# Optimization experiments

Measured on AMD Instinct MI355X. Metric: run time of the kernel, lower is better.

Reference implementation:

```python
import jax, jax.numpy as jnp
import numpy as np

N = 8192   # num_nodes
H = 128    # hidden_dim
B = 100    # batch of events
K = 5      # num_neg_samples
TD_MAX = 10000.0
TIME_SD = jnp.array([50.0, 7.0, 15.0, 15.0])  # time_sd from forward; time_mean = 0


def setup_inputs() -> dict:
    key = jax.random.key(0)
    ks = jax.random.split(key, 16)
    p = 32.0 / N  # avg degree ~32
    A = (jax.random.uniform(ks[0], (N, N)) < p).astype(jnp.float32)
    # S init: S[v,u] = 1/D[v] for neighbors u (row-normalized A)
    S = A / (A.sum(axis=1, keepdims=True) + 1e-7)
    z0 = jax.random.normal(ks[1], (N, H)) * 0.1
    u = jax.random.randint(ks[2], (B,), 0, N)
    v = jax.random.randint(ks[3], (B,), 0, N)
    event_types = jax.random.randint(ks[4], (B,), 0, 2)
    neg_idx = jax.random.randint(ks[5], (B, 2 * K), 0, N)
    time_diff = jax.random.normal(ks[6], (B, 2, 4))
    t_bar = jax.random.uniform(ks[7], (B, N)) * 1000.0
    t = 1000.0 + 10.0 * jnp.arange(B, dtype=jnp.float32)

    def lin(k, o, i):
        k1, k2 = jax.random.split(k)
        lim = 1.0 / np.sqrt(i)
        return (jax.random.uniform(k1, (o, i), minval=-lim, maxval=lim),
                jax.random.uniform(k2, (o,), minval=-lim, maxval=lim))

    om0_w, om0_b = lin(ks[8], 1, 2 * H)
    om1_w, om1_b = lin(ks[9], 1, 2 * H)
    Wh_w, Wh_b = lin(ks[10], H, H)
    Ws_w, Ws_b = lin(ks[11], H, H)
    Wr_w, Wr_b = lin(ks[12], H, H)
    Wt_w, Wt_b = lin(ks[13], H, 4)
    return dict(u=u, v=v, event_types=event_types, neg_idx=neg_idx,
                time_diff=time_diff, t_bar=t_bar, t=t, z0=z0, A=A, S=S,
                w_t=0.5 * jnp.ones(2), alpha=0.5 * jnp.ones(2), psi=0.5 * jnp.ones(2),
                om0_w=om0_w, om0_b=om0_b, om1_w=om1_w, om1_b=om1_b,
                Wh_w=Wh_w, Wh_b=Wh_b, Ws_w=Ws_w, Ws_b=Ws_b,
                Wr_w=Wr_w, Wr_b=Wr_b, Wt_w=Wt_w, Wt_b=Wt_b)


def _forward(u, v, event_types, neg_idx, time_diff, t_bar, t, z0, A, S,
             w_t, alpha, psi, om0_w, om0_b, om1_w, om1_b,
             Wh_w, Wh_b, Ws_w, Ws_b, Wr_w, Wr_b, Wt_w, Wt_b):
    td_norm = time_diff / TIME_SD  # (td - 0) / sd

    def hawkes(zu, zv, et, td):
        # lambda = psi * log(1 + exp(g/psi)) + alpha * exp(-w_t * td/td_max)
        zc = jnp.concatenate([zu, zv], axis=-1)
        g0 = jnp.einsum('...d,d->...', zc, om0_w[0]) + om0_b[0]
        g1 = jnp.einsum('...d,d->...', zc, om1_w[0]) + om1_b[0]
        g = jnp.where(et == 0, g0, g1)
        ps, al, wt = psi[et], alpha[et], w_t[et]
        gp = jnp.clip(g / (ps + 1e-7), -75.0, 75.0)
        return ps * jnp.log1p(jnp.exp(gp)) + al * jnp.exp(-wt * (td / TD_MAX))

    ar = jnp.arange(N)

    def step(z, ev):
        u_it, v_it, et, td2, tb, t_it, neg = ev
        z_u, z_v = z[u_it], z[v_it]
        Wh_all = z @ Wh_w.T + Wh_b  # [N,H]

        def struct(node):
            # structural attention over node's neighbors (masked, not dense loop)
            mask = A[node] > 0
            q = jnp.exp(S[node]) * mask
            q = q / (q.sum() + 1e-7)
            hsig = jax.nn.sigmoid(q[:, None] * Wh_all)
            hmax = jnp.where(mask[:, None], hsig, -jnp.inf).max(axis=0)
            return jnp.where(jnp.any(mask), hmax, 0.0)

        # update of u uses struct info from v's neighborhood, and vice versa
        hs = jnp.stack([struct(v_it), struct(u_it)])  # [2,H]
        h = (hs @ Ws_w.T + Ws_b) + (jnp.stack([z_u, z_v]) @ Wr_w.T + Wr_b) + (td2 @ Wt_w.T + Wt_b)
        z_upd = jax.nn.sigmoid(h)
        z_new = z.at[u_it].set(z_upd[0]).at[v_it].set(z_upd[1])

        # negative pairs: (u, v_neg_k) then (u_neg_k, v), using z_prev
        v_neg, u_neg = neg[:K], neg[K:]
        zu_neg = jnp.concatenate([jnp.broadcast_to(z_u, (K, H)), z[u_neg]], 0)
        zv_neg = jnp.concatenate([z[v_neg], jnp.broadcast_to(z_v, (K, H))], 0)
        lt_u = jnp.concatenate([jnp.full((K,), tb[u_it]), tb[u_neg]])
        lt_v = jnp.concatenate([tb[v_neg], jnp.full((K,), tb[v_it])])
        ts_neg = t_it - jnp.maximum(lt_u, lt_v)
        ts_pos = t_it - jnp.maximum(tb[u_it], tb[v_it])

        # all-node intensity prediction (Lambda_dict path, detached in torch)
        zd = jax.lax.stop_gradient(z)
        zu_all = jnp.concatenate([jnp.broadcast_to(jax.lax.stop_gradient(z_u), (N, H)),
                                  jnp.broadcast_to(jax.lax.stop_gradient(z_v), (N, H))], 0)
        zv_all = jnp.concatenate([zd, zd], 0)
        last_t = jnp.maximum(
            jnp.concatenate([jnp.full((N,), tb[u_it]), jnp.full((N,), tb[v_it])]),
            jnp.concatenate([tb, tb]))
        lam_all = hawkes(zu_all, zv_all, jnp.full((2 * N,), et),
                         jax.lax.stop_gradient(t_it - last_t))
        m = ((ar != u_it) & (ar != v_it)).astype(lam_all.dtype)
        lam_sum = jax.lax.stop_gradient(jnp.sum(lam_all * jnp.concatenate([m, m])))

        return z_new, (z_u, z_v, zu_neg, zv_neg, ts_pos, ts_neg, lam_sum)

    _, (zu_p, zv_p, zun, zvn, ts_p, ts_n, lam_sums) = jax.lax.scan(
        step, z0, (u, v, event_types, td_norm, t_bar, t, neg_idx))

    lam_pos = hawkes(zu_p, zv_p, event_types, ts_p)            # [B]
    lam_neg = hawkes(zun, zvn, event_types[:, None], ts_n)      # [B,2K]
    return jnp.concatenate([lam_pos[:, None], lam_neg, lam_sums[:, None]], axis=1)  # [B, 2K+2]


def reference(u, v, event_types, neg_idx, time_diff, t_bar, t, z0, A, S,
              w_t, alpha, psi, om0_w, om0_b, om1_w, om1_b,
              Wh_w, Wh_b, Ws_w, Ws_b, Wr_w, Wr_b, Wt_w, Wt_b):
    return _forward(u, v, event_types, neg_idx, time_diff, t_bar, t, z0, A, S,
                    w_t, alpha, psi, om0_w, om0_b, om1_w, om1_b,
                    Wh_w, Wh_b, Ws_w, Ws_b, Wr_w, Wr_b, Wt_w, Wt_b)
```

## Files before the change

### kernel.cpp

```cpp
#include <hip/hip_runtime.h>
#include <math.h>

#define N 8192
#define H 128
#define BB 100
#define KK 5
#define MAXN 256
#define TD_MAXF 10000.0f

#define OFF_WHALLV ((size_t)N * H)
#define OFF_ZVER (OFF_WHALLV + 2 * BB * H)

#define AGENT_LD(p) \
  __hip_atomic_load((p), __ATOMIC_RELAXED, __HIP_MEMORY_SCOPE_AGENT)
#define AGENT_ST(p, v) \
  __hip_atomic_store((p), (v), __ATOMIC_RELAXED, __HIP_MEMORY_SCOPE_AGENT)

__global__ __launch_bounds__(256) void prep_kernel(
    const float* __restrict__ Wh, const float* __restrict__ Ws,
    const float* __restrict__ Wr, const float* __restrict__ z0,
    const float* __restrict__ om0, const float* __restrict__ om1,
    float* __restrict__ WhT, float* __restrict__ WsT, float* __restrict__ WrT,
    float* __restrict__ dvec0, unsigned* __restrict__ done) {
  const int B0 = H * H, B1 = 2 * H * H, B2 = 3 * H * H;
  const int B3 = B2 + 4;
  int idx = blockIdx.x * 256 + threadIdx.x;
  if (idx < B0) {
    int d = idx >> 7, k = idx & (H - 1);
    WhT[k * H + d] = Wh[d * H + k];
  } else if (idx < B1) {
    int e = idx - B0;
    int d = e >> 7, k = e & (H - 1);
    WsT[k * H + d] = Ws[d * H + k];
  } else if (idx < B2) {
    int e = idx - B1;
    int d = e >> 7, k = e & (H - 1);
    WrT[k * H + d] = Wr[d * H + k];
  } else if (idx < B3) {
    AGENT_ST(&done[idx - B2], 0u);
  } else if (idx < B3 + N) {
    int j = idx - B3;
    const float4* zr = (const float4*)(z0 + (size_t)j * H);
    const float4* o0 = (const float4*)om0;
    const float4* o1 = (const float4*)om1;
    float a0 = 0, b0 = 0, a1 = 0, b1 = 0;
    for (int k = 0; k < H / 4; ++k) {
      float4 zv = zr[k];
      float4 l0 = o0[k], r0 = o0[k + H / 4];
      float4 l1 = o1[k], r1 = o1[k + H / 4];
      a0 += zv.x * l0.x + zv.y * l0.y + zv.z * l0.z + zv.w * l0.w;
      b0 += zv.x * r0.x + zv.y * r0.y + zv.z * r0.z + zv.w * r0.w;
      a1 += zv.x * l1.x + zv.y * l1.y + zv.z * l1.z + zv.w * l1.w;
      b1 += zv.x * r1.x + zv.y * r1.y + zv.z * r1.z + zv.w * r1.w;
    }
    dvec0[0 * N + j] = a0;
    dvec0[1 * N + j] = b0;
    dvec0[2 * N + j] = a1;
    dvec0[3 * N + j] = b1;
  }
}

__global__ __launch_bounds__(256) void whall_kernel(
    const float* __restrict__ z0, const float* __restrict__ WhT,
    const float* __restrict__ Wh_b, float* __restrict__ whall) {
  const int blk = blockIdx.x;
  const int tid = threadIdx.x;
  __shared__ float zr2[2][H];
  int r = tid >> 7, d = tid & (H - 1);
  int row = blk * 2 + r;
  zr2[r][d] = z0[(size_t)row * H + d];
  __syncthreads();
  float acc = Wh_b[d];
#pragma unroll 8
  for (int k = 0; k < H; ++k) acc += zr2[r][k] * WhT[k * H + d];
  whall[(size_t)row * H + d] = acc;
}

__global__ __launch_bounds__(1024, 4) void fused_kernel(
    const int* __restrict__ u_, const int* __restrict__ v_,
    const int* __restrict__ et_, const int* __restrict__ neg_,
    const float* __restrict__ time_diff, const float* __restrict__ t_bar,
    const float* __restrict__ tt, const float* __restrict__ z0,
    const float* __restrict__ A, const float* __restrict__ S,
    const float* __restrict__ WhT, const float* __restrict__ WsT,
    const float* __restrict__ WrT, const float* __restrict__ Wh_b,
    const float* __restrict__ Ws_b, const float* __restrict__ Wr_b,
    const float* __restrict__ Wt_w, const float* __restrict__ Wt_b,
    const float* __restrict__ w_t, const float* __restrict__ alpha,
    const float* __restrict__ psi, const float* __restrict__ om0_w,
    const float* __restrict__ om1_w, const float* __restrict__ om0_b,
    const float* __restrict__ om1_b, const float* __restrict__ wsf,
    float* __restrict__ zver, float* __restrict__ whallv,
    float* __restrict__ dlog, const float* __restrict__ dvec0,
    unsigned* done, float* __restrict__ out) {
  const int blk = blockIdx.x;
  const int t = threadIdx.x;
  __shared__ float scratch[8][2][H];
  __shared__ float hsS[2][H];
  __shared__ float zrowS[2][H];
  __shared__ float zupdS[2][H];
  __shared__ float td2S[2][4];
  __shared__ int nidxS[2][MAXN];
  __shared__ float nqS[2][MAXN];
  __shared__ int woffS[2][MAXN];
  __shared__ int cMS[2];
  __shared__ int zsrcS[2];
  __shared__ unsigned needS[4];
  __shared__ int uL[BB], vL[BB];
  __shared__ int wsumI[16];
  __shared__ float wsumF[16];
  __shared__ float dR[N];
  __shared__ float red[1024];
  __shared__ float suS, svS;

  if (blk < BB) {
    const int b = blk;
    const int r = t >> 9;
    const int tr = t & 511;
    const int sub = (t >> 7) & 3;
    const int d = t & (H - 1);
    const int ks = t >> 7;
    const int k0 = ks * 16;

    if (t < BB) {
      uL[t] = u_[t];
      vL[t] = v_[t];
    }
    if (t >= 512 && t < 520) {
      int i = t - 512;
      int cc = i & 3;
      float sd = (cc == 0) ? 50.0f : ((cc == 1) ? 7.0f : 15.0f);
      td2S[i >> 2][cc] = time_diff[b * 8 + i] / sd;
    }
    if (t >= 1020) needS[t - 1020] = 0u;
    const float whb = Wh_b[d];
    float wsReg[16], wrReg[16], whReg[16];
#pragma unroll
    for (int kk = 0; kk < 16; ++kk) {
      wsReg[kk] = WsT[(k0 + kk) * H + d];
      wrReg[kk] = WrT[(k0 + kk) * H + d];
      whReg[kk] = WhT[(k0 + kk) * H + d];
    }
    float biasReg = 0.0f;
    float4 wt4Reg = {0.0f, 0.0f, 0.0f, 0.0f};
    if (t < 256) {
      int dd = t & (H - 1);
      biasReg = Ws_b[dd] + Wr_b[dd] + Wt_b[dd];
      wt4Reg = ((const float4*)Wt_w)[dd];
    }
    float omA = 0.0f, omB = 0.0f;
    if (t >= 256 && t < 768) {
      int w = (t - 256) >> 6;
      int lane6 = t & 63;
      int which = w & 3;
      int wsel = which >> 1;
      int offo = (which & 1) * H;
      const float* omw = wsel ? om1_w : om0_w;
      omA = omw[offo + lane6];
      omB = omw[offo + 64 + lane6];
    }

    const int node = r ? u_[b] : v_[b];
    unsigned hm = 0u;
    int c = 0;
    float local = 0.0f;
    for (int it = 0; it < N / 512; ++it) {
      int j = it * 512 + tr;
      if (A[(size_t)node * N + j] > 0.0f) {
        hm |= 1u << it;
        ++c;
        local += expf(S[(size_t)node * N + j]);
      }
    }
    const int lane = t & 63;
    const int wv = t >> 6;
    int ex = c;
    for (int s2 = 1; s2 < 64; s2 <<= 1) {
      int o = __shfl_up(ex, s2);
      if (lane >= s2) ex += o;
    }
    float ls = local;
    for (int s2 = 32; s2 > 0; s2 >>= 1) ls += __shfl_down(ls, s2);
    if (lane == 63) wsumI[wv] = ex;
    if (lane == 0) wsumF[wv] = ls;
    ex -= c;
    __syncthreads();

    int base0 = 0, ctot = 0;
    float qs = 0.0f;
    {
      int w0 = r * 8;
#pragma unroll
      for (int w = 0; w < 8; ++w) {
        int wi = w0 + w;
        int cw = wsumI[wi];
        if (wi < wv) base0 += cw;
        ctot += cw;
        qs += wsumF[wi];
      }
    }
    const float iq = 1.0f / (qs + 1e-7f);
    int p = base0 + ex;
    for (int it = 0; it < N / 512; ++it) {
      if ((hm >> it) & 1u) {
        int j = it * 512 + tr;
        if (p < MAXN) {
          nidxS[r][p] = j;
          nqS[r][p] = expf(S[(size_t)node * N + j]);
        }
        ++p;
      }
    }
    const int cM = min(ctot, MAXN);
    if (tr == 0) cMS[r] = cM;
    __syncthreads();

    for (int i = tr; i < cM; i += 512) {
      int n = nidxS[r][i];
      int a = -1, row = 0;
      for (int s2 = b - 1; s2 >= 0; --s2) {
        if (vL[s2] == n) { a = s2; row = 1; break; }
        if (uL[s2] == n) { a = s2; row = 0; break; }
      }
      woffS[r][i] = (a < 0) ? n * H : (int)OFF_WHALLV + (2 * a + row) * H;
      nqS[r][i] *= iq;
      if (a >= 0) atomicOr(&needS[a >> 5], 1u << (a & 31));
    }
    if (t < 2) {
      int nd = t ? vL[b] : uL[b];
      int a = -1, row = 0;
      for (int s2 = b - 1; s2 >= 0; --s2) {
        if (vL[s2] == nd) { a = s2; row = 1; break; }
        if (uL[s2] == nd) { a = s2; row = 0; break; }
      }
      zsrcS[t] = (a >= 0) ? 2 * a + row : -1;
      if (a >= 0) atomicOr(&needS[a >> 5], 1u << (a & 31));
    }
    __syncthreads();

    float zpre = 0.0f;
    int zs = -1;
    if (t < 256) {
      int rr = t >> 7, dd = t & (H - 1);
      zs = zsrcS[rr];
      if (zs < 0) {
        int nd = rr ? vL[b] : uL[b];
        zpre = z0[(size_t)nd * H + dd];
      }
    }

    float mx = -INFINITY;
    for (int i = sub; i < cM; i += 4) {
      int off = woffS[r][i];
      if (off < (int)OFF_WHALLV)
        mx = fmaxf(mx, nqS[r][i] * wsf[(size_t)off + d]);
    }
    if (t == 0) {
      for (int w = 0; w < 4; ++w) {
        unsigned nw = needS[w];
        if (!nw) continue;
        while ((AGENT_LD(&done[w]) & nw) != nw) __builtin_amdgcn_s_sleep(1);
      }
    }
    __syncthreads();

    const int ub = uL[b], vb = vL[b];

    for (int i = sub; i < cM; i += 4) {
      int off = woffS[r][i];
      if (off >= (int)OFF_WHALLV)
        mx = fmaxf(mx, nqS[r][i] * AGENT_LD(&wsf[(size_t)off + d]));
    }
    scratch[sub][r][d] = mx;
    if (t < 256) {
      int rr = t >> 7, dd = t & (H - 1);
      zrowS[rr][dd] =
          (zs < 0) ? zpre : AGENT_LD(&wsf[OFF_ZVER + (size_t)zs * H + dd]);
    }
    __syncthreads();

    if (t < 2 * H) {
      int rr = t >> 7, dd = t & (H - 1);
      float m = fmaxf(fmaxf(scratch[0][rr][dd], scratch[1][rr][dd]),
                      fmaxf(scratch[2][rr][dd], scratch[3][rr][dd]));
      hsS[rr][dd] = (cMS[rr] > 0) ? (1.0f / (1.0f + expf(-m))) : 0.0f;
    }
    __syncthreads();

    {
      float a0 = 0.0f, a1 = 0.0f;
#pragma unroll
      for (int kk = 0; kk < 16; ++kk) {
        int k = k0 + kk;
        a0 += hsS[0][k] * wsReg[kk] + zrowS[0][k] * wrReg[kk];
        a1 += hsS[1][k] * wsReg[kk] + zrowS[1][k] * wrReg[kk];
      }
      scratch[ks][0][d] = a0;
      scratch[ks][1][d] = a1;
    }
    __syncthreads();

    if (t < 2 * H) {
      int rr = t >> 7, dd = t & (H - 1);
      float acc = biasReg;
#pragma unroll
      for (int kx = 0; kx < 8; ++kx) acc += scratch[kx][rr][dd];
      acc += td2S[rr][0] * wt4Reg.x + td2S[rr][1] * wt4Reg.y +
             td2S[rr][2] * wt4Reg.z + td2S[rr][3] * wt4Reg.w;
      float zu = 1.0f / (1.0f + expf(-acc));
      zupdS[rr][dd] = zu;
      AGENT_ST(&zver[(size_t)(2 * b + rr) * H + dd], zu);
    }
    __syncthreads();

    {
      int r0 = (ub == vb) ? 1 : 0;
      float f0 = 0.0f, f1 = 0.0f;
#pragma unroll
      for (int kk = 0; kk < 16; ++kk) {
        int k = k0 + kk;
        f0 += zupdS[r0][k] * whReg[kk];
        f1 += zupdS[1][k] * whReg[kk];
      }
      scratch[ks][0][d] = f0;
      scratch[ks][1][d] = f1;
    }
    __syncthreads();

    if (t < 2 * H) {
      int rr = t >> 7, dd = t & (H - 1);
      float acc = whb;
#pragma unroll
      for (int kx = 0; kx < 8; ++kx) acc += scratch[kx][rr][dd];
      AGENT_ST(&whallv[(size_t)(2 * b + rr) * H + dd], acc);
    } else if (t < 768) {
      int w = (t - 256) >> 6;
      int lane6 = t & 63;
      int row = w >> 2;
      int which = w & 3;
      int rr = (row == 0 && ub == vb) ? 1 : row;
      float val = zupdS[rr][lane6] * omA + zupdS[rr][64 + lane6] * omB;
      for (int s2 = 32; s2 > 0; s2 >>= 1) val += __shfl_down(val, s2);
      if (lane6 == 0) AGENT_ST(&dlog[b * 8 + which * 2 + row], val);
    }
    __syncthreads();

    if (t == 0) {
      asm volatile("s_waitcnt vmcnt(0)" ::: "memory");
      __hip_atomic_fetch_or(&done[b >> 5], 1u << (b & 31), __ATOMIC_RELAXED,
                            __HIP_MEMORY_SCOPE_AGENT);
    }
    return;
  }

  const int b = blk - BB;
  const int e = et_[b];
  const int ub = u_[b], vb = v_[b];
  const float ps = psi[e], al = alpha[e], wt = w_t[e];
  const float ob0 = om0_b[0], ob1 = om1_b[0];
  const float ob = e ? ob1 : ob0;
  const float tcur = tt[b];
  const float inv_ps = 1.0f / (ps + 1e-7f);
  const int whichR = 2 * e + 1;
  const int whichL = 2 * e;

  if (t < BB) {
    uL[t] = u_[t];
    vL[t] = v_[t];
  }
  {
    const float4* base = (const float4*)(dvec0 + (size_t)whichR * N);
    float4* dst = (float4*)dR;
    for (int i = t; i < N / 4; i += 1024) dst[i] = base[i];
  }
  if (t == 0) {
    for (int w = 0; w < 4; ++w) {
      int cb = b - 32 * w;
      unsigned nw =
          (cb >= 32) ? 0xffffffffu : (cb <= 0 ? 0u : ((1u << cb) - 1u));
      if (!nw) continue;
      while ((AGENT_LD(&done[w]) & nw) != nw) __builtin_amdgcn_s_sleep(1);
    }
  }
  __syncthreads();

  for (int i = t; i < b; i += 1024) {
    int ui = uL[i], vi = vL[i];
    bool u_over = (ui == vi);
    bool v_over = false;
    for (int j = i + 1; j < b; ++j) {
      int uj = uL[j], vj = vL[j];
      u_over = u_over || (uj == ui) || (vj == ui);
      v_over = v_over || (uj == vi) || (vj == vi);
    }
    if (!u_over) dR[ui] = AGENT_LD(&dlog[i * 8 + whichR * 2 + 0]);
    if (!v_over) dR[vi] = AGENT_LD(&dlog[i * 8 + whichR * 2 + 1]);
  }

  if (t < 13) {
    auto dpre = [&](int x, int which) -> float {
      for (int bp = b - 1; bp >= 0; --bp) {
        if (vL[bp] == x) return AGENT_LD(&dlog[bp * 8 + which * 2 + 1]);
        if (uL[bp] == x) return AGENT_LD(&dlog[bp * 8 + which * 2 + 0]);
      }
      return dvec0[(size_t)which * N + x];
    };
    if (t < 11) {
      int li, ri;
      float ltu, ltv;
      if (t == 0) {
        li = ub; ri = vb;
        ltu = t_bar[(size_t)b * N + ub];
        ltv = t_bar[(size_t)b * N + vb];
      } else if (t <= 5) {
        int vn = neg_[b * (2 * KK) + (t - 1)];
        li = ub; ri = vn;
        ltu = t_bar[(size_t)b * N + ub];
        ltv = t_bar[(size_t)b * N + vn];
      } else {
        int un = neg_[b * (2 * KK) + (t - 1)];
        li = un; ri = vb;
        ltu = t_bar[(size_t)b * N + un];
        ltv = t_bar[(size_t)b * N + vb];
      }
      float g = dpre(li, whichL) + dpre(ri, whichR) + ob;
      float gp = fminf(fmaxf(g * inv_ps, -75.0f), 75.0f);
      float ts = tcur - fmaxf(ltu, ltv);
      out[b * 12 + t] = ps * log1pf(expf(gp)) + al * expf(-wt * (ts / TD_MAXF));
    } else if (t == 11) {
      suS = dpre(ub, whichL);
    } else {
      svS = dpre(vb, whichL);
    }
  }
  __syncthreads();

  const float su = suS, sv = svS;
  const float tb_u = t_bar[(size_t)b * N + ub];
  const float tb_v = t_bar[(size_t)b * N + vb];
  const float Ku = expf((su + ob) * inv_ps);
  const float Kv = expf((sv + ob) * inv_ps);
  const float Cx = al * expf(-wt * (tcur / TD_MAXF));
  const float Eu = expf(wt * (tb_u / TD_MAXF));
  const float Ev = expf(wt * (tb_v / TD_MAXF));
  const float wTD = wt / TD_MAXF;
  const float4* tb4 = (const float4*)(t_bar + (size_t)b * N);
  const float4* dR4 = (const float4*)dR;
  float acc = 0.0f;
  for (int j4 = t; j4 < N / 4; j4 += 1024) {
    float4 dv = dR4[j4];
    float4 tb = tb4[j4];
    float de[4] = {dv.x, dv.y, dv.z, dv.w};
    float te[4] = {tb.x, tb.y, tb.z, tb.w};
#pragma unroll
    for (int ee = 0; ee < 4; ++ee) {
      int j = j4 * 4 + ee;
      if (j == ub || j == vb) continue;
      float Dj = expf(de[ee] * inv_ps);
      float spl = ps * (log1pf(Ku * Dj) + log1pf(Kv * Dj));
      float Ej = expf(wTD * te[ee]);
      float ex2 = Cx * (fmaxf(Eu, Ej) + fmaxf(Ev, Ej));
      acc += spl + ex2;
    }
  }
  red[t] = acc;
  __syncthreads();
  for (int s2 = 512; s2 > 0; s2 >>= 1) {
    if (t < s2) red[t] += red[t + s2];
    __syncthreads();
  }
  if (t == 0) out[b * 12 + 11] = red[0];
}

extern "C" void kernel_launch(void* const* d_in, const int* in_sizes, int n_in,
                              void* d_out, int out_size, void* d_ws,
                              size_t ws_size, hipStream_t stream) {
  const int* u = (const int*)d_in[0];
  const int* v = (const int*)d_in[1];
  const int* et = (const int*)d_in[2];
  const int* neg = (const int*)d_in[3];
  const float* time_diff = (const float*)d_in[4];
  const float* t_bar = (const float*)d_in[5];
  const float* t = (const float*)d_in[6];
  const float* z0 = (const float*)d_in[7];
  const float* A = (const float*)d_in[8];
  const float* S = (const float*)d_in[9];
  const float* w_t = (const float*)d_in[10];
  const float* alpha = (const float*)d_in[11];
  const float* psi = (const float*)d_in[12];
  const float* om0_w = (const float*)d_in[13];
  const float* om0_b = (const float*)d_in[14];
  const float* om1_w = (const float*)d_in[15];
  const float* om1_b = (const float*)d_in[16];
  const float* Wh_w = (const float*)d_in[17];
  const float* Wh_b = (const float*)d_in[18];
  const float* Ws_w = (const float*)d_in[19];
  const float* Ws_b = (const float*)d_in[20];
  const float* Wr_w = (const float*)d_in[21];
  const float* Wr_b = (const float*)d_in[22];
  const float* Wt_w = (const float*)d_in[23];
  const float* Wt_b = (const float*)d_in[24];
  float* out = (float*)d_out;

  float* wsf = (float*)d_ws;
  float* whall = wsf;
  float* whallv = wsf + OFF_WHALLV;
  float* zver = wsf + OFF_ZVER;
  float* WhT = zver + 2 * BB * H;
  float* WsT = WhT + H * H;
  float* WrT = WsT + H * H;
  float* dvec0 = WrT + H * H;
  float* dlog = dvec0 + 4 * N;
  unsigned* done = (unsigned*)(dlog + 8 * BB);

  const int PREP_ELEMS = 3 * H * H + 4 + N;
  prep_kernel<<<(PREP_ELEMS + 255) / 256, 256, 0, stream>>>(
      Wh_w, Ws_w, Wr_w, z0, om0_w, om1_w, WhT, WsT, WrT, dvec0, done);
  whall_kernel<<<N / 2, 256, 0, stream>>>(z0, WhT, Wh_b, whall);
  fused_kernel<<<2 * BB, 1024, 0, stream>>>(
      u, v, et, neg, time_diff, t_bar, t, z0, A, S, WhT, WsT, WrT, Wh_b,
      Ws_b, Wr_b, Wt_w, Wt_b, w_t, alpha, psi, om0_w, om1_w, om0_b, om1_b,
      wsf, zver, whallv, dlog, dvec0, done, out);
}
```

Before: 583.7 us.

## Replace packed done bitmask with per-event staged ready flags on separate lines

The single bitmask word per 32 events is replaced by per-event flags spaced 32 words apart. Each event block now signals three stages: zver ready, whallv ready, and dlog ready. Consumers wait, in parallel across threads, only on the stage they need, so a dependent block can start as soon as the zver it needs is written instead of waiting for the producer to finish completely. The A row loads are also hoisted into registers so they are all issued before the count loop. The cost is more flag stores and fences per block, plus many threads polling at once.

Result: no change. 576.6 us (-1.2%).

```diff
diff --git a/kernel.cpp b/kernel.cpp
--- a/kernel.cpp
+++ b/kernel.cpp
@@ -7,6 +7,7 @@
 #define KK 5
 #define MAXN 256
 #define TD_MAXF 10000.0f
+#define RDLINE 32
 
 #define OFF_WHALLV ((size_t)N * H)
 #define OFF_ZVER (OFF_WHALLV + 2 * BB * H)
@@ -21,9 +22,9 @@
     const float* __restrict__ Wr, const float* __restrict__ z0,
     const float* __restrict__ om0, const float* __restrict__ om1,
     float* __restrict__ WhT, float* __restrict__ WsT, float* __restrict__ WrT,
-    float* __restrict__ dvec0, unsigned* __restrict__ done) {
+    float* __restrict__ dvec0, unsigned* __restrict__ ready) {
   const int B0 = H * H, B1 = 2 * H * H, B2 = 3 * H * H;
-  const int B3 = B2 + 4;
+  const int B3 = B2 + BB * RDLINE;
   int idx = blockIdx.x * 256 + threadIdx.x;
   if (idx < B0) {
     int d = idx >> 7, k = idx & (H - 1);
@@ -37,7 +38,7 @@
     int d = e >> 7, k = e & (H - 1);
     WrT[k * H + d] = Wr[d * H + k];
   } else if (idx < B3) {
-    AGENT_ST(&done[idx - B2], 0u);
+    AGENT_ST(&ready[idx - B2], 0u);
   } else if (idx < B3 + N) {
     int j = idx - B3;
     const float4* zr = (const float4*)(z0 + (size_t)j * H);
@@ -92,7 +93,7 @@
     const float* __restrict__ om1_b, const float* __restrict__ wsf,
     float* __restrict__ zver, float* __restrict__ whallv,
     float* __restrict__ dlog, const float* __restrict__ dvec0,
-    unsigned* done, float* __restrict__ out) {
+    unsigned* ready, float* __restrict__ out) {
   const int blk = blockIdx.x;
   const int t = threadIdx.x;
   __shared__ float scratch[8][2][H];
@@ -105,7 +106,7 @@
   __shared__ int woffS[2][MAXN];
   __shared__ int cMS[2];
   __shared__ int zsrcS[2];
-  __shared__ unsigned needS[4];
+  __shared__ int needP[BB];
   __shared__ int uL[BB], vL[BB];
   __shared__ int wsumI[16];
   __shared__ float wsumF[16];
@@ -125,6 +126,7 @@
     if (t < BB) {
       uL[t] = u_[t];
       vL[t] = v_[t];
+      needP[t] = 0;
     }
     if (t >= 512 && t < 520) {
       int i = t - 512;
@@ -132,7 +134,6 @@
       float sd = (cc == 0) ? 50.0f : ((cc == 1) ? 7.0f : 15.0f);
       td2S[i >> 2][cc] = time_diff[b * 8 + i] / sd;
     }
-    if (t >= 1020) needS[t - 1020] = 0u;
     const float whb = Wh_b[d];
     float wsReg[16], wrReg[16], whReg[16];
 #pragma unroll
@@ -161,15 +162,19 @@
     }
 
     const int node = r ? u_[b] : v_[b];
+    float aReg[16];
+#pragma unroll
+    for (int it = 0; it < 16; ++it)
+      aReg[it] = A[(size_t)node * N + it * 512 + tr];
     unsigned hm = 0u;
     int c = 0;
     float local = 0.0f;
-    for (int it = 0; it < N / 512; ++it) {
-      int j = it * 512 + tr;
-      if (A[(size_t)node * N + j] > 0.0f) {
+#pragma unroll
+    for (int it = 0; it < 16; ++it) {
+      if (aReg[it] > 0.0f) {
         hm |= 1u << it;
         ++c;
-        local += expf(S[(size_t)node * N + j]);
+        local += expf(S[(size_t)node * N + it * 512 + tr]);
       }
     }
     const int lane = t & 63;
@@ -201,7 +206,7 @@
     }
     const float iq = 1.0f / (qs + 1e-7f);
     int p = base0 + ex;
-    for (int it = 0; it < N / 512; ++it) {
+    for (int it = 0; it < 16; ++it) {
       if ((hm >> it) & 1u) {
         int j = it * 512 + tr;
         if (p < MAXN) {
@@ -224,7 +229,7 @@
       }
       woffS[r][i] = (a < 0) ? n * H : (int)OFF_WHALLV + (2 * a + row) * H;
       nqS[r][i] *= iq;
-      if (a >= 0) atomicOr(&needS[a >> 5], 1u << (a & 31));
+      if (a >= 0) needP[a] = 1;
     }
     if (t < 2) {
       int nd = t ? vL[b] : uL[b];
@@ -234,7 +239,6 @@
         if (uL[s2] == nd) { a = s2; row = 0; break; }
       }
       zsrcS[t] = (a >= 0) ? 2 * a + row : -1;
-      if (a >= 0) atomicOr(&needS[a >> 5], 1u << (a & 31));
     }
     __syncthreads();
 
@@ -255,11 +259,19 @@
       if (off < (int)OFF_WHALLV)
         mx = fmaxf(mx, nqS[r][i] * wsf[(size_t)off + d]);
     }
-    if (t == 0) {
-      for (int w = 0; w < 4; ++w) {
-        unsigned nw = needS[w];
-        if (!nw) continue;
-        while ((AGENT_LD(&done[w]) & nw) != nw) __builtin_amdgcn_s_sleep(1);
+    {
+      const unsigned* paddr = nullptr;
+      if (t < BB) {
+        if (needP[t]) paddr = &ready[t * RDLINE + 0];
+      } else if (t == 512) {
+        int zz = zsrcS[0];
+        if (zz >= 0) paddr = &ready[(zz >> 1) * RDLINE + 1];
+      } else if (t == 513) {
+        int zz = zsrcS[1];
+        if (zz >= 0) paddr = &ready[(zz >> 1) * RDLINE + 1];
+      }
+      if (paddr) {
+        while (AGENT_LD(paddr) == 0u) __builtin_amdgcn_s_sleep(8);
       }
     }
     __syncthreads();
@@ -312,6 +324,10 @@
       AGENT_ST(&zver[(size_t)(2 * b + rr) * H + dd], zu);
     }
     __syncthreads();
+    if (t == 0) {
+      asm volatile("s_waitcnt vmcnt(0)" ::: "memory");
+      AGENT_ST(&ready[b * RDLINE + 1], 1u);
+    }
 
     {
       int r0 = (ub == vb) ? 1 : 0;
@@ -333,7 +349,14 @@
 #pragma unroll
       for (int kx = 0; kx < 8; ++kx) acc += scratch[kx][rr][dd];
       AGENT_ST(&whallv[(size_t)(2 * b + rr) * H + dd], acc);
-    } else if (t < 768) {
+    }
+    __syncthreads();
+    if (t == 0) {
+      asm volatile("s_waitcnt vmcnt(0)" ::: "memory");
+      AGENT_ST(&ready[b * RDLINE + 0], 1u);
+    }
+
+    if (t >= 256 && t < 768) {
       int w = (t - 256) >> 6;
       int lane6 = t & 63;
       int row = w >> 2;
@@ -344,11 +367,9 @@
       if (lane6 == 0) AGENT_ST(&dlog[b * 8 + which * 2 + row], val);
     }
     __syncthreads();
-
     if (t == 0) {
       asm volatile("s_waitcnt vmcnt(0)" ::: "memory");
-      __hip_atomic_fetch_or(&done[b >> 5], 1u << (b & 31), __ATOMIC_RELAXED,
-                            __HIP_MEMORY_SCOPE_AGENT);
+      AGENT_ST(&ready[b * RDLINE + 2], 1u);
     }
     return;
   }
@@ -373,14 +394,9 @@
     float4* dst = (float4*)dR;
     for (int i = t; i < N / 4; i += 1024) dst[i] = base[i];
   }
-  if (t == 0) {
-    for (int w = 0; w < 4; ++w) {
-      int cb = b - 32 * w;
-      unsigned nw =
-          (cb >= 32) ? 0xffffffffu : (cb <= 0 ? 0u : ((1u << cb) - 1u));
-      if (!nw) continue;
-      while ((AGENT_LD(&done[w]) & nw) != nw) __builtin_amdgcn_s_sleep(1);
-    }
+  if (t < b) {
+    const unsigned* pa = &ready[t * RDLINE + 2];
+    while (AGENT_LD(pa) == 0u) __builtin_amdgcn_s_sleep(8);
   }
   __syncthreads();
 
@@ -511,14 +527,14 @@
   float* WrT = WsT + H * H;
   float* dvec0 = WrT + H * H;
   float* dlog = dvec0 + 4 * N;
-  unsigned* done = (unsigned*)(dlog + 8 * BB);
-
-  const int PREP_ELEMS = 3 * H * H + 4 + N;
+  unsigned* ready = (unsigned*)(dlog + 8 * BB);
+
+  const int PREP_ELEMS = 3 * H * H + BB * RDLINE + N;
   prep_kernel<<<(PREP_ELEMS + 255) / 256, 256, 0, stream>>>(
-      Wh_w, Ws_w, Wr_w, z0, om0_w, om1_w, WhT, WsT, WrT, dvec0, done);
+      Wh_w, Ws_w, Wr_w, z0, om0_w, om1_w, WhT, WsT, WrT, dvec0, ready);
   whall_kernel<<<N / 2, 256, 0, stream>>>(z0, WhT, Wh_b, whall);
   fused_kernel<<<2 * BB, 1024, 0, stream>>>(
       u, v, et, neg, time_diff, t_bar, t, z0, A, S, WhT, WsT, WrT, Wh_b,
       Ws_b, Wr_b, Wt_w, Wt_b, w_t, alpha, psi, om0_w, om1_w, om0_b, om1_b,
-      wsf, zver, whallv, dlog, dvec0, done, out);
+      wsf, zver, whallv, dlog, dvec0, ready, out);
 }
```
